# Kernel tuning notes

Measured on AMD Instinct MI355X. Metric: run time of the kernel, lower is better.

## Reference

```python
import jax, jax.numpy as jnp
import numpy as np

N_NODES = 50000
N_EDGES = 500000
F_IN = 128
HIDDEN = 128
N_CLASSES = 32
N_GRAPHS = 64


def setup_inputs() -> dict:
    key = jax.random.key(0)
    ks = jax.random.split(key, 16)
    x = jax.random.normal(ks[0], (N_NODES, F_IN), dtype=jnp.float32)
    edge_index = jax.random.randint(ks[1], (2, N_EDGES), 0, N_NODES, dtype=jnp.int64)
    batch = jnp.sort(jax.random.randint(ks[2], (N_NODES,), 0, N_GRAPHS, dtype=jnp.int64))
    d = {"x": x, "edge_index": edge_index, "batch": batch}
    dims = [(F_IN, HIDDEN)] + [(HIDDEN, HIDDEN)] * 4
    for i, (fi, fo) in enumerate(dims, start=1):
        s = 1.0 / np.sqrt(fi)
        d[f"W{i}"] = jax.random.uniform(ks[2 + i], (fi, fo), jnp.float32, -s, s)
        d[f"b{i}"] = jnp.zeros((fo,), jnp.float32)
    s = 1.0 / np.sqrt(HIDDEN)
    d["W_lin"] = jax.random.uniform(ks[10], (HIDDEN, N_CLASSES), jnp.float32, -s, s)
    d["b_lin"] = jnp.zeros((N_CLASSES,), jnp.float32)
    return d


def _gcn_conv(x, W, b, src, dst, norm_edge, norm_self):
    # PyG GCNConv: h = x @ W; out[dst] += norm * h[src]; + self-loop + bias
    h = x @ W
    msg = h[src] * norm_edge[:, None]                      # [E, F] gather + scale
    agg = jax.ops.segment_sum(msg, dst, num_segments=x.shape[0])  # scatter-add
    return agg + h * norm_self[:, None] + b


def reference(x, edge_index, batch, W1, b1, W2, b2, W3, b3, W4, b4, W5, b5, W_lin, b_lin):
    src, dst = edge_index[0], edge_index[1]
    n = x.shape[0]
    # degree with self-loops (in-degree at dst, +1 for the self loop)
    deg = jax.ops.segment_sum(jnp.ones_like(dst, dtype=x.dtype), dst, num_segments=n) + 1.0
    dis = jax.lax.rsqrt(deg)
    norm_edge = dis[src] * dis[dst]   # per-edge symmetric normalization
    norm_self = dis * dis             # self-loop coefficient = 1/deg

    h = jax.nn.relu(_gcn_conv(x, W1, b1, src, dst, norm_edge, norm_self))
    h = jax.nn.relu(_gcn_conv(h, W2, b2, src, dst, norm_edge, norm_self))
    h = jax.nn.relu(_gcn_conv(h, W3, b3, src, dst, norm_edge, norm_self))
    h = jax.nn.relu(_gcn_conv(h, W4, b4, src, dst, norm_edge, norm_self))
    h = _gcn_conv(h, W5, b5, src, dst, norm_edge, norm_self)

    # global mean pool over graphs in the batch
    sums = jax.ops.segment_sum(h, batch, num_segments=N_GRAPHS)
    counts = jax.ops.segment_sum(jnp.ones((n,), h.dtype), batch, num_segments=N_GRAPHS)
    pooled = sums / jnp.maximum(counts, 1.0)[:, None]
    # dropout is identity in eval mode
    return pooled @ W_lin + b_lin
```

## Files before the change

kernel.cpp:

```cpp
#include <hip/hip_runtime.h>
#include <hip/hip_bf16.h>

#define N_NODES   50000
#define N_EDGES   500000
#define FDIM      128
#define N_CLASSES 32
#define N_GRAPHS  64


__global__ void deg_kernel(const int* __restrict__ dst, int* __restrict__ deg, int E) {
    int e = blockIdx.x * blockDim.x + threadIdx.x;
    if (e < E) atomicAdd(&deg[dst[e]], 1);
}

__global__ void scan_partial(const int* __restrict__ deg, int* __restrict__ part,
                             float* __restrict__ dis, int n) {
    __shared__ int s[512];
    int t = threadIdx.x;
    int i = blockIdx.x * 512 + t;
    int d = (i < n) ? deg[i] : 0;
    if (i < n) dis[i] = rsqrtf((float)d + 1.0f);
    s[t] = (i < n) ? ((d + 3) & ~3) : 0;
    __syncthreads();
    for (int o = 256; o > 0; o >>= 1) {
        if (t < o) s[t] += s[t + o];
        __syncthreads();
    }
    if (t == 0) part[blockIdx.x] = s[0];
}

__global__ void scan_offsets(int* part, int nb) {
    if (blockIdx.x == 0 && threadIdx.x == 0) {
        int acc = 0;
        for (int i = 0; i < nb; i++) { int v = part[i]; part[i] = acc; acc += v; }
    }
}

__global__ void scan_final(const int* __restrict__ deg, const int* __restrict__ part,
                           int* __restrict__ rowptr, int n) {
    __shared__ int s[512];
    int t = threadIdx.x;
    int i = blockIdx.x * 512 + t;
    int v = (i < n) ? ((deg[i] + 3) & ~3) : 0;
    s[t] = v;
    __syncthreads();
    for (int o = 1; o < 512; o <<= 1) {
        int x = (t >= o) ? s[t - o] : 0;
        __syncthreads();
        s[t] += x;
        __syncthreads();
    }
    if (i < n) rowptr[i] = part[blockIdx.x] + s[t] - v;
}

__global__ void fill_csr(const int* __restrict__ src, const int* __restrict__ dst,
                         const int* __restrict__ rowptr, int* __restrict__ fill,
                         const float* __restrict__ dis,
                         int2* __restrict__ csr_sw, int E) {
    int e = blockIdx.x * blockDim.x + threadIdx.x;
    if (e >= E) return;
    int d = dst[e], s = src[e];
    int pos = rowptr[d] + atomicAdd(&fill[d], 1);
    float w = dis[s] * dis[d];
    csr_sw[pos] = make_int2(s, __float_as_int(w));
}

__global__ void pad_csr(const int* __restrict__ deg, const int* __restrict__ rowptr,
                        int2* __restrict__ csr_sw, int n) {
    int v = blockIdx.x * blockDim.x + threadIdx.x;
    if (v >= n) return;
    int d = deg[v], dp = (d + 3) & ~3;
    int base = rowptr[v];
    for (int i = d; i < dp; i++) csr_sw[base + i] = make_int2(v, 0);
}


__global__ __launch_bounds__(256) void gemm32(const float* __restrict__ X,
                                              const float* __restrict__ W,
                                              float* __restrict__ H, int n) {
    __shared__ __align__(16) float xs[32][36];
    __shared__ __align__(16) float ws[32][132];
    int t = threadIdx.x;
    int ti = t & 7;
    int tj = t >> 3;
    int rowBase = blockIdx.x * 32;

    float acc[4][4];
#pragma unroll
    for (int r = 0; r < 4; r++)
#pragma unroll
        for (int c = 0; c < 4; c++) acc[r][c] = 0.f;

    for (int k0 = 0; k0 < 128; k0 += 32) {
        __syncthreads();
        {
            int r = t >> 3, kq = t & 7;
            int grow = rowBase + r;
            float4 v = make_float4(0.f, 0.f, 0.f, 0.f);
            if (grow < n) v = *(const float4*)(X + (size_t)grow * FDIM + k0 + kq * 4);
            xs[kq * 4 + 0][r] = v.x;
            xs[kq * 4 + 1][r] = v.y;
            xs[kq * 4 + 2][r] = v.z;
            xs[kq * 4 + 3][r] = v.w;
        }
        {
            int c4 = t & 31, kr = t >> 5;
#pragma unroll
            for (int p = 0; p < 4; p++) {
                int k = kr + 8 * p;
                float4 v = *(const float4*)(W + (size_t)(k0 + k) * FDIM + c4 * 4);
                *(float4*)&ws[k][c4 * 4] = v;
            }
        }
        __syncthreads();
#pragma unroll 8
        for (int k = 0; k < 32; k++) {
            float4 a = *(const float4*)&xs[k][ti * 4];
            float4 b = *(const float4*)&ws[k][tj * 4];
            float ar[4] = {a.x, a.y, a.z, a.w};
            float br[4] = {b.x, b.y, b.z, b.w};
#pragma unroll
            for (int r = 0; r < 4; r++)
#pragma unroll
                for (int c = 0; c < 4; c++) acc[r][c] = fmaf(ar[r], br[c], acc[r][c]);
        }
    }

#pragma unroll
    for (int rr = 0; rr < 4; rr++) {
        int grow = rowBase + ti * 4 + rr;
        if (grow < n) {
            float4 o = {acc[rr][0], acc[rr][1], acc[rr][2], acc[rr][3]};
            *(float4*)(H + (size_t)grow * FDIM + tj * 4) = o;
        }
    }
}


#define PGATH(I, EBASE)                                                         \
    int2 p##I = sw[(EBASE) + 2 * (I) + half];                                   \
    float4 m##I = *(const float4*)(H + (size_t)p##I.x * FDIM + q * 4);

#define PFMA(I)                                                                 \
    {                                                                           \
        float w_ = __int_as_float(p##I.y);                                      \
        acc.x = fmaf(w_, m##I.x, acc.x);                                        \
        acc.y = fmaf(w_, m##I.y, acc.y);                                        \
        acc.z = fmaf(w_, m##I.z, acc.z);                                        \
        acc.w = fmaf(w_, m##I.w, acc.w);                                        \
    }

__global__ __launch_bounds__(256) void agg_kernel(const float* __restrict__ H,
                                                  float* __restrict__ OUT,
                                                  const int* __restrict__ rowptr,
                                                  const int* __restrict__ degi,
                                                  const int2* __restrict__ csr_sw,
                                                  const float* __restrict__ dis,
                                                  const float* __restrict__ bias,
                                                  int n, int relu) {
    int wid = (blockIdx.x * blockDim.x + threadIdx.x) >> 6;
    int lane = threadIdx.x & 63;
    if (wid >= n) return;
    int v = __builtin_amdgcn_readfirstlane(wid);
    int half = lane >> 5;
    int q = lane & 31;

    const int2* sw = csr_sw + rowptr[v];
    int cnt = (degi[v] + 3) & ~3;
    float4 acc = make_float4(0.f, 0.f, 0.f, 0.f);
    int e = 0;

    for (; e + 16 <= cnt; e += 16) {
        PGATH(0, e) PGATH(1, e) PGATH(2, e) PGATH(3, e)
        PGATH(4, e) PGATH(5, e) PGATH(6, e) PGATH(7, e)
        PFMA(0) PFMA(1) PFMA(2) PFMA(3) PFMA(4) PFMA(5) PFMA(6) PFMA(7)
    }
    if (e + 8 <= cnt) {
        PGATH(0, e) PGATH(1, e) PGATH(2, e) PGATH(3, e)
        PFMA(0) PFMA(1) PFMA(2) PFMA(3)
        e += 8;
    }
    if (e + 4 <= cnt) {
        PGATH(0, e) PGATH(1, e)
        PFMA(0) PFMA(1)
    }

    acc.x += __shfl_xor(acc.x, 32);
    acc.y += __shfl_xor(acc.y, 32);
    acc.z += __shfl_xor(acc.z, 32);
    acc.w += __shfl_xor(acc.w, 32);

    if (half == 0) {
        float dv = dis[v];
        float ns = dv * dv;
        float4 hv = *(const float4*)(H + (size_t)v * FDIM + q * 4);
        float4 bb = *(const float4*)(bias + q * 4);
        float4 o;
        o.x = acc.x + ns * hv.x + bb.x;
        o.y = acc.y + ns * hv.y + bb.y;
        o.z = acc.z + ns * hv.z + bb.z;
        o.w = acc.w + ns * hv.w + bb.w;
        if (relu) {
            o.x = fmaxf(o.x, 0.f); o.y = fmaxf(o.y, 0.f);
            o.z = fmaxf(o.z, 0.f); o.w = fmaxf(o.w, 0.f);
        }
        *(float4*)(OUT + (size_t)v * FDIM + q * 4) = o;
    }
}


#define POOL_BLOCKS 1024

__global__ __launch_bounds__(128) void pool_kernel(const float* __restrict__ H,
                                                   const int* __restrict__ batch,
                                                   float* __restrict__ psum,
                                                   float* __restrict__ pcnt, int n) {
    int t = threadIdx.x;
    int chunk = (n + POOL_BLOCKS - 1) / POOL_BLOCKS;
    int lo = blockIdx.x * chunk;
    int hi = lo + chunk; if (hi > n) hi = n;
    if (lo >= hi) return;

    float acc = 0.f;
    int cnt = 0;
    int curg = batch[lo];
    float hv = H[(size_t)lo * FDIM + t];
    int g = curg;
    for (int v = lo; v < hi; v++) {
        float hcur = hv;
        int gcur = g;
        if (v + 1 < hi) {
            hv = H[(size_t)(v + 1) * FDIM + t];
            g = batch[v + 1];
        }
        if (gcur != curg) {
            atomicAdd(&psum[curg * FDIM + t], acc);
            if (t == 0) atomicAdd(&pcnt[curg], (float)cnt);
            acc = 0.f; cnt = 0; curg = gcur;
        }
        acc += hcur;
        cnt++;
    }
    atomicAdd(&psum[curg * FDIM + t], acc);
    if (t == 0) atomicAdd(&pcnt[curg], (float)cnt);
}

__global__ void final_lin(const float* __restrict__ psum, const float* __restrict__ pcnt,
                          const float* __restrict__ Wl, const float* __restrict__ bl,
                          float* __restrict__ out) {
    int t = blockIdx.x * blockDim.x + threadIdx.x;
    if (t >= N_GRAPHS * N_CLASSES) return;
    int g = t >> 5, c = t & 31;
    float inv = 1.0f / fmaxf(pcnt[g], 1.0f);
    float s = 0.f;
    for (int k = 0; k < FDIM; k++) s = fmaf(psum[g * FDIM + k], Wl[k * N_CLASSES + c], s);
    out[t] = s * inv + bl[c];
}


static inline size_t align256(size_t x) { return (x + 255) & ~(size_t)255; }

extern "C" void kernel_launch(void* const* d_in, const int* in_sizes, int n_in,
                              void* d_out, int out_size, void* d_ws, size_t ws_size,
                              hipStream_t stream) {
    const float* x     = (const float*)d_in[0];
    const int*   ei    = (const int*)d_in[1];
    const int*   batch = (const int*)d_in[2];
    const float* Wls[5] = {(const float*)d_in[3], (const float*)d_in[5], (const float*)d_in[7],
                           (const float*)d_in[9], (const float*)d_in[11]};
    const float* bls[5] = {(const float*)d_in[4], (const float*)d_in[6], (const float*)d_in[8],
                           (const float*)d_in[10], (const float*)d_in[12]};
    const float* W_lin = (const float*)d_in[13];
    const float* b_lin = (const float*)d_in[14];
    float* out = (float*)d_out;

    const int N = N_NODES, E = N_EDGES;
    const int* src = ei;
    const int* dst = ei + E;

    char* p = (char*)d_ws;
    size_t off = 0;
    float* hA = (float*)(p + off); off = align256(off + (size_t)N * FDIM * 4);
    float* hB = (float*)(p + off); off = align256(off + (size_t)N * FDIM * 4);
    int2*  csr_sw = (int2*)(p + off); off = align256(off + ((size_t)E + 4 * N) * 8);
    float* dis = (float*)(p + off); off = align256(off + (size_t)N * 4);
    int*   rowptr = (int*)(p + off); off = align256(off + (size_t)N * 4);
    int*   part = (int*)(p + off); off = align256(off + 512);
    size_t zero_off = off;
    int*   deg = (int*)(p + off); off = align256(off + (size_t)N * 4);
    int*   fill = (int*)(p + off); off = align256(off + (size_t)N * 4);
    float* psum = (float*)(p + off); off = align256(off + (size_t)N_GRAPHS * FDIM * 4);
    float* pcnt = (float*)(p + off); off = align256(off + (size_t)N_GRAPHS * 4);
    size_t zero_bytes = off - zero_off;
    (void)ws_size; (void)n_in; (void)in_sizes; (void)out_size;

    hipMemsetAsync(p + zero_off, 0, zero_bytes, stream);

    deg_kernel<<<(E + 255) / 256, 256, 0, stream>>>(dst, deg, E);
    int nChunks = (N + 511) / 512;
    scan_partial<<<nChunks, 512, 0, stream>>>(deg, part, dis, N);
    scan_offsets<<<1, 64, 0, stream>>>(part, nChunks);
    scan_final<<<nChunks, 512, 0, stream>>>(deg, part, rowptr, N);
    fill_csr<<<(E + 255) / 256, 256, 0, stream>>>(src, dst, rowptr, fill, dis,
                                                  csr_sw, E);
    pad_csr<<<(N + 255) / 256, 256, 0, stream>>>(deg, rowptr, csr_sw, N);

    int gemmBlocks = (N + 31) / 32;
    int aggBlocks = (N * 64 + 255) / 256;
    const float* cur = x;
    for (int l = 0; l < 5; l++) {
        gemm32<<<gemmBlocks, 256, 0, stream>>>(cur, Wls[l], hA, N);
        int relu = (l < 4) ? 1 : 0;
        agg_kernel<<<aggBlocks, 256, 0, stream>>>(hA, hB, rowptr, deg, csr_sw,
                                                  dis, bls[l], N, relu);
        cur = hB;
    }

    pool_kernel<<<POOL_BLOCKS, 128, 0, stream>>>(hB, batch, psum, pcnt, N);
    final_lin<<<(N_GRAPHS * N_CLASSES + 255) / 256, 256, 0, stream>>>(psum, pcnt, W_lin,
                                                                      b_lin, out);
}
```

Before: 450.2 us.

## Fuse aggregation and GEMM per layer by aggregating before the weight multiply

```diff
diff --git a/kernel.cpp b/kernel.cpp
--- a/kernel.cpp
+++ b/kernel.cpp
@@ -75,68 +75,6 @@
 }
 
 
-__global__ __launch_bounds__(256) void gemm32(const float* __restrict__ X,
-                                              const float* __restrict__ W,
-                                              float* __restrict__ H, int n) {
-    __shared__ __align__(16) float xs[32][36];
-    __shared__ __align__(16) float ws[32][132];
-    int t = threadIdx.x;
-    int ti = t & 7;
-    int tj = t >> 3;
-    int rowBase = blockIdx.x * 32;
-
-    float acc[4][4];
-#pragma unroll
-    for (int r = 0; r < 4; r++)
-#pragma unroll
-        for (int c = 0; c < 4; c++) acc[r][c] = 0.f;
-
-    for (int k0 = 0; k0 < 128; k0 += 32) {
-        __syncthreads();
-        {
-            int r = t >> 3, kq = t & 7;
-            int grow = rowBase + r;
-            float4 v = make_float4(0.f, 0.f, 0.f, 0.f);
-            if (grow < n) v = *(const float4*)(X + (size_t)grow * FDIM + k0 + kq * 4);
-            xs[kq * 4 + 0][r] = v.x;
-            xs[kq * 4 + 1][r] = v.y;
-            xs[kq * 4 + 2][r] = v.z;
-            xs[kq * 4 + 3][r] = v.w;
-        }
-        {
-            int c4 = t & 31, kr = t >> 5;
-#pragma unroll
-            for (int p = 0; p < 4; p++) {
-                int k = kr + 8 * p;
-                float4 v = *(const float4*)(W + (size_t)(k0 + k) * FDIM + c4 * 4);
-                *(float4*)&ws[k][c4 * 4] = v;
-            }
-        }
-        __syncthreads();
-#pragma unroll 8
-        for (int k = 0; k < 32; k++) {
-            float4 a = *(const float4*)&xs[k][ti * 4];
-            float4 b = *(const float4*)&ws[k][tj * 4];
-            float ar[4] = {a.x, a.y, a.z, a.w};
-            float br[4] = {b.x, b.y, b.z, b.w};
-#pragma unroll
-            for (int r = 0; r < 4; r++)
-#pragma unroll
-                for (int c = 0; c < 4; c++) acc[r][c] = fmaf(ar[r], br[c], acc[r][c]);
-        }
-    }
-
-#pragma unroll
-    for (int rr = 0; rr < 4; rr++) {
-        int grow = rowBase + ti * 4 + rr;
-        if (grow < n) {
-            float4 o = {acc[rr][0], acc[rr][1], acc[rr][2], acc[rr][3]};
-            *(float4*)(H + (size_t)grow * FDIM + tj * 4) = o;
-        }
-    }
-}
-
-
 #define PGATH(I, EBASE)                                                         \
     int2 p##I = sw[(EBASE) + 2 * (I) + half];                                   \
     float4 m##I = *(const float4*)(H + (size_t)p##I.x * FDIM + q * 4);
@@ -150,61 +88,115 @@
         acc.w = fmaf(w_, m##I.w, acc.w);                                        \
     }
 
-__global__ __launch_bounds__(256) void agg_kernel(const float* __restrict__ H,
-                                                  float* __restrict__ OUT,
-                                                  const int* __restrict__ rowptr,
-                                                  const int* __restrict__ degi,
-                                                  const int2* __restrict__ csr_sw,
-                                                  const float* __restrict__ dis,
-                                                  const float* __restrict__ bias,
-                                                  int n, int relu) {
-    int wid = (blockIdx.x * blockDim.x + threadIdx.x) >> 6;
-    int lane = threadIdx.x & 63;
-    if (wid >= n) return;
-    int v = __builtin_amdgcn_readfirstlane(wid);
+__global__ __launch_bounds__(256) void fused_layer(const float* __restrict__ H,
+                                                   const float* __restrict__ W,
+                                                   const float* __restrict__ bias,
+                                                   float* __restrict__ OUT,
+                                                   const int* __restrict__ rowptr,
+                                                   const int* __restrict__ degi,
+                                                   const int2* __restrict__ csr_sw,
+                                                   const float* __restrict__ dis,
+                                                   int n, int relu) {
+    __shared__ __align__(16) float xs[FDIM][36];
+    __shared__ __align__(16) float ws[32][132];
+    int t = threadIdx.x;
+    int lane = t & 63;
+    int wv = t >> 6;
     int half = lane >> 5;
     int q = lane & 31;
-
-    const int2* sw = csr_sw + rowptr[v];
-    int cnt = (degi[v] + 3) & ~3;
-    float4 acc = make_float4(0.f, 0.f, 0.f, 0.f);
-    int e = 0;
-
-    for (; e + 16 <= cnt; e += 16) {
-        PGATH(0, e) PGATH(1, e) PGATH(2, e) PGATH(3, e)
-        PGATH(4, e) PGATH(5, e) PGATH(6, e) PGATH(7, e)
-        PFMA(0) PFMA(1) PFMA(2) PFMA(3) PFMA(4) PFMA(5) PFMA(6) PFMA(7)
-    }
-    if (e + 8 <= cnt) {
-        PGATH(0, e) PGATH(1, e) PGATH(2, e) PGATH(3, e)
-        PFMA(0) PFMA(1) PFMA(2) PFMA(3)
-        e += 8;
-    }
-    if (e + 4 <= cnt) {
-        PGATH(0, e) PGATH(1, e)
-        PFMA(0) PFMA(1)
-    }
-
-    acc.x += __shfl_xor(acc.x, 32);
-    acc.y += __shfl_xor(acc.y, 32);
-    acc.z += __shfl_xor(acc.z, 32);
-    acc.w += __shfl_xor(acc.w, 32);
-
-    if (half == 0) {
-        float dv = dis[v];
-        float ns = dv * dv;
-        float4 hv = *(const float4*)(H + (size_t)v * FDIM + q * 4);
-        float4 bb = *(const float4*)(bias + q * 4);
-        float4 o;
-        o.x = acc.x + ns * hv.x + bb.x;
-        o.y = acc.y + ns * hv.y + bb.y;
-        o.z = acc.z + ns * hv.z + bb.z;
-        o.w = acc.w + ns * hv.w + bb.w;
-        if (relu) {
-            o.x = fmaxf(o.x, 0.f); o.y = fmaxf(o.y, 0.f);
-            o.z = fmaxf(o.z, 0.f); o.w = fmaxf(o.w, 0.f);
-        }
-        *(float4*)(OUT + (size_t)v * FDIM + q * 4) = o;
+    int rowBase = blockIdx.x * 32;
+
+    for (int i = 0; i < 8; i++) {
+        int r = wv * 8 + i;
+        int v = rowBase + r;
+        float4 acc = make_float4(0.f, 0.f, 0.f, 0.f);
+        if (v < n) {
+            const int2* sw = csr_sw + rowptr[v];
+            int cnt = (degi[v] + 3) & ~3;
+            int e = 0;
+            for (; e + 16 <= cnt; e += 16) {
+                PGATH(0, e) PGATH(1, e) PGATH(2, e) PGATH(3, e)
+                PGATH(4, e) PGATH(5, e) PGATH(6, e) PGATH(7, e)
+                PFMA(0) PFMA(1) PFMA(2) PFMA(3) PFMA(4) PFMA(5) PFMA(6) PFMA(7)
+            }
+            if (e + 8 <= cnt) {
+                PGATH(0, e) PGATH(1, e) PGATH(2, e) PGATH(3, e)
+                PFMA(0) PFMA(1) PFMA(2) PFMA(3)
+                e += 8;
+            }
+            if (e + 4 <= cnt) {
+                PGATH(0, e) PGATH(1, e)
+                PFMA(0) PFMA(1)
+            }
+            acc.x += __shfl_xor(acc.x, 32);
+            acc.y += __shfl_xor(acc.y, 32);
+            acc.z += __shfl_xor(acc.z, 32);
+            acc.w += __shfl_xor(acc.w, 32);
+            float dv = dis[v];
+            float ns = dv * dv;
+            float4 hv = *(const float4*)(H + (size_t)v * FDIM + q * 4);
+            acc.x = fmaf(ns, hv.x, acc.x);
+            acc.y = fmaf(ns, hv.y, acc.y);
+            acc.z = fmaf(ns, hv.z, acc.z);
+            acc.w = fmaf(ns, hv.w, acc.w);
+        }
+        if (half == 0) {
+            xs[q * 4 + 0][r] = acc.x;
+            xs[q * 4 + 1][r] = acc.y;
+            xs[q * 4 + 2][r] = acc.z;
+            xs[q * 4 + 3][r] = acc.w;
+        }
+    }
+
+    int ti = t & 7;
+    int tj = t >> 3;
+    float acc2[4][4];
+#pragma unroll
+    for (int r = 0; r < 4; r++)
+#pragma unroll
+        for (int c = 0; c < 4; c++) acc2[r][c] = 0.f;
+
+    for (int k0 = 0; k0 < 128; k0 += 32) {
+        __syncthreads();
+        {
+            int c4 = t & 31, kr = t >> 5;
+#pragma unroll
+            for (int p = 0; p < 4; p++) {
+                int k = kr + 8 * p;
+                float4 v = *(const float4*)(W + (size_t)(k0 + k) * FDIM + c4 * 4);
+                *(float4*)&ws[k][c4 * 4] = v;
+            }
+        }
+        __syncthreads();
+#pragma unroll 8
+        for (int k = 0; k < 32; k++) {
+            float4 a = *(const float4*)&xs[k0 + k][ti * 4];
+            float4 b = *(const float4*)&ws[k][tj * 4];
+            float ar[4] = {a.x, a.y, a.z, a.w};
+            float br[4] = {b.x, b.y, b.z, b.w};
+#pragma unroll
+            for (int r = 0; r < 4; r++)
+#pragma unroll
+                for (int c = 0; c < 4; c++) acc2[r][c] = fmaf(ar[r], br[c], acc2[r][c]);
+        }
+    }
+
+    float4 bb = *(const float4*)(bias + tj * 4);
+#pragma unroll
+    for (int rr = 0; rr < 4; rr++) {
+        int grow = rowBase + ti * 4 + rr;
+        if (grow < n) {
+            float4 o;
+            o.x = acc2[rr][0] + bb.x;
+            o.y = acc2[rr][1] + bb.y;
+            o.z = acc2[rr][2] + bb.z;
+            o.w = acc2[rr][3] + bb.w;
+            if (relu) {
+                o.x = fmaxf(o.x, 0.f); o.y = fmaxf(o.y, 0.f);
+                o.z = fmaxf(o.z, 0.f); o.w = fmaxf(o.w, 0.f);
+            }
+            *(float4*)(OUT + (size_t)grow * FDIM + tj * 4) = o;
+        }
     }
 }
 
@@ -305,18 +297,18 @@
                                                   csr_sw, E);
     pad_csr<<<(N + 255) / 256, 256, 0, stream>>>(deg, rowptr, csr_sw, N);
 
-    int gemmBlocks = (N + 31) / 32;
-    int aggBlocks = (N * 64 + 255) / 256;
+    int fusedBlocks = (N + 31) / 32;
     const float* cur = x;
+    float* bufs[2] = {hA, hB};
     for (int l = 0; l < 5; l++) {
-        gemm32<<<gemmBlocks, 256, 0, stream>>>(cur, Wls[l], hA, N);
+        float* dst_h = bufs[l & 1];
         int relu = (l < 4) ? 1 : 0;
-        agg_kernel<<<aggBlocks, 256, 0, stream>>>(hA, hB, rowptr, deg, csr_sw,
-                                                  dis, bls[l], N, relu);
-        cur = hB;
-    }
-
-    pool_kernel<<<POOL_BLOCKS, 128, 0, stream>>>(hB, batch, psum, pcnt, N);
+        fused_layer<<<fusedBlocks, 256, 0, stream>>>(cur, Wls[l], bls[l], dst_h,
+                                                     rowptr, deg, csr_sw, dis, N, relu);
+        cur = dst_h;
+    }
+
+    pool_kernel<<<POOL_BLOCKS, 128, 0, stream>>>(hA, batch, psum, pcnt, N);
     final_lin<<<(N_GRAPHS * N_CLASSES + 255) / 256, 256, 0, stream>>>(psum, pcnt, W_lin,
                                                                       b_lin, out);
 }
```

New measurement: 419.7 us. 6.8% less time.
